# Kernel tuning notes

Hardware: AMD Instinct MI355X
Metric: run time of the kernel (lower is better)

Reference implementation:

```python
import jax, jax.numpy as jnp
import numpy as np
from jax import lax

B, T, D, NH = 8, 2048, 128, 4
HD = D // NH
EPS = 1e-5


def _ln(x, g, b):
    m = x.mean(-1, keepdims=True)
    v = ((x - m) ** 2).mean(-1, keepdims=True)
    return (x - m) / jnp.sqrt(v + EPS) * g + b


def _gelu(x):  # exact (erf) GELU, matching torch nn.GELU default
    return jax.nn.gelu(x, approximate=False)


def _forward(lob_feat, trade_feat, has_trade,
             ei_w, ei_b, ei_g, ei_beta, decay,
             in_proj_w, in_proj_b, out_proj_w, out_proj_b,
             cn_g, cn_b,
             lob_w, lob_b, lob_g, lob_beta,
             tr_w, tr_b, tr_g, tr_beta,
             of_w, of_b, of_g, of_beta):
    # event impact: Linear -> LayerNorm -> Tanh, gated by has_trade
    impact = jnp.tanh(_ln(trade_feat @ ei_w.T + ei_b, ei_g, ei_beta))
    impact = impact * has_trade[..., None]              # [B,T,D]

    # diagonal linear recurrence: state_t = sigmoid(decay) * state_{t-1} + impact_t
    d = jax.nn.sigmoid(decay)                           # [D]

    def step(s, x):
        s = d * s + x
        return s, s

    _, states = lax.scan(step, jnp.zeros_like(impact[:, 0]),
                         jnp.swapaxes(impact, 0, 1))    # [T,B,D]
    state_seq = jnp.swapaxes(states, 0, 1)              # [B,T,D]

    # fusion MLPs (dropout is identity in eval)
    lob_enh = _gelu(_ln(jnp.concatenate([lob_feat, state_seq], -1) @ lob_w.T + lob_b,
                        lob_g, lob_beta))
    trade_enh = _gelu(_ln(jnp.concatenate([trade_feat, state_seq], -1) @ tr_w.T + tr_b,
                          tr_g, tr_beta))

    # torch nn.MultiheadAttention (batch_first): q=lob_enh, k=v=trade_enh
    wq, wk, wv = in_proj_w[:D], in_proj_w[D:2 * D], in_proj_w[2 * D:]
    bq, bk, bv = in_proj_b[:D], in_proj_b[D:2 * D], in_proj_b[2 * D:]
    q = (lob_enh @ wq.T + bq).reshape(B, T, NH, HD)
    k = (trade_enh @ wk.T + bk).reshape(B, T, NH, HD)
    v = (trade_enh @ wv.T + bv).reshape(B, T, NH, HD)
    scores = jnp.einsum('bqhd,bkhd->bhqk', q, k) / jnp.sqrt(jnp.float32(HD))
    attn = jax.nn.softmax(scores, axis=-1)
    ctx = jnp.einsum('bhqk,bkhd->bqhd', attn, v).reshape(B, T, D)
    fused_attn = ctx @ out_proj_w.T + out_proj_b

    fused = _ln(lob_enh + fused_attn, cn_g, cn_b)
    output = _gelu(_ln(jnp.concatenate([fused, trade_enh], -1) @ of_w.T + of_b,
                       of_g, of_beta))
    return output


def setup_inputs() -> dict:
    key = jax.random.key(0)
    ks = jax.random.split(key, 20)
    s1 = 1.0 / np.sqrt(D)
    s2 = 1.0 / np.sqrt(2 * D)
    return {
        'lob_feat': jax.random.normal(ks[0], (B, T, D), jnp.float32),
        'trade_feat': jax.random.normal(ks[1], (B, T, D), jnp.float32),
        'has_trade': (jax.random.uniform(ks[2], (B, T)) < 0.5).astype(jnp.float32),
        'ei_w': jax.random.normal(ks[3], (D, D), jnp.float32) * s1,
        'ei_b': jnp.zeros((D,), jnp.float32),
        'ei_g': jnp.ones((D,), jnp.float32),
        'ei_beta': jnp.zeros((D,), jnp.float32),
        'decay': jnp.ones((D,), jnp.float32) * 0.9,
        'in_proj_w': jax.random.normal(ks[4], (3 * D, D), jnp.float32) * s1,
        'in_proj_b': jnp.zeros((3 * D,), jnp.float32),
        'out_proj_w': jax.random.normal(ks[5], (D, D), jnp.float32) * s1,
        'out_proj_b': jnp.zeros((D,), jnp.float32),
        'cn_g': jnp.ones((D,), jnp.float32),
        'cn_b': jnp.zeros((D,), jnp.float32),
        'lob_w': jax.random.normal(ks[6], (D, 2 * D), jnp.float32) * s2,
        'lob_b': jnp.zeros((D,), jnp.float32),
        'lob_g': jnp.ones((D,), jnp.float32),
        'lob_beta': jnp.zeros((D,), jnp.float32),
        'tr_w': jax.random.normal(ks[7], (D, 2 * D), jnp.float32) * s2,
        'tr_b': jnp.zeros((D,), jnp.float32),
        'tr_g': jnp.ones((D,), jnp.float32),
        'tr_beta': jnp.zeros((D,), jnp.float32),
        'of_w': jax.random.normal(ks[8], (D, 2 * D), jnp.float32) * s2,
        'of_b': jnp.zeros((D,), jnp.float32),
        'of_g': jnp.ones((D,), jnp.float32),
        'of_beta': jnp.zeros((D,), jnp.float32),
    }


def reference(lob_feat, trade_feat, has_trade,
              ei_w, ei_b, ei_g, ei_beta, decay,
              in_proj_w, in_proj_b, out_proj_w, out_proj_b,
              cn_g, cn_b,
              lob_w, lob_b, lob_g, lob_beta,
              tr_w, tr_b, tr_g, tr_beta,
              of_w, of_b, of_g, of_beta):
    return _forward(lob_feat, trade_feat, has_trade,
                    ei_w, ei_b, ei_g, ei_beta, decay,
                    in_proj_w, in_proj_b, out_proj_w, out_proj_b,
                    cn_g, cn_b,
                    lob_w, lob_b, lob_g, lob_beta,
                    tr_w, tr_b, tr_g, tr_beta,
                    of_w, of_b, of_g, of_beta)
```

## Files before the change

kernel.cpp:

```cpp
#include <hip/hip_runtime.h>
#include <math.h>


#define T_  2048

typedef short bf16x8 __attribute__((ext_vector_type(8)));
typedef float f32x4  __attribute__((ext_vector_type(4)));
typedef unsigned short ushort_t;

__device__ __forceinline__ float sigm(float x) { return 1.0f / (1.0f + __expf(-x)); }

__device__ __forceinline__ unsigned short f2bf(float x) {
    union { float f; unsigned u; } v; v.f = x;
    unsigned r = v.u + 0x7FFFu + ((v.u >> 16) & 1u);
    return (unsigned short)(r >> 16);
}

__global__ __launch_bounds__(256) void prep_kernel(
    const float* __restrict__ lob, const float* __restrict__ trade,
    const float* __restrict__ eiw, const float* __restrict__ ipw,
    const float* __restrict__ opw, const float* __restrict__ lobw,
    const float* __restrict__ trw, const float* __restrict__ ofw,
    ushort_t* __restrict__ pool)
{
    const size_t i8 = ((size_t)blockIdx.x * 256 + threadIdx.x) * 8;
    const float* src; size_t off;
    if      (i8 < 2097152) { src = lob;   off = 0; }
    else if (i8 < 4194304) { src = trade; off = 2097152; }
    else if (i8 < 4210688) { src = eiw;   off = 4194304; }
    else if (i8 < 4259840) { src = ipw;   off = 4210688; }
    else if (i8 < 4276224) { src = opw;   off = 4259840; }
    else if (i8 < 4308992) { src = lobw;  off = 4276224; }
    else if (i8 < 4341760) { src = trw;   off = 4308992; }
    else                   { src = ofw;   off = 4341760; }
    const float4 a = *(const float4*)(src + (i8 - off));
    const float4 b = *(const float4*)(src + (i8 - off) + 4);
    bf16x8 o;
    o[0] = (short)f2bf(a.x); o[1] = (short)f2bf(a.y);
    o[2] = (short)f2bf(a.z); o[3] = (short)f2bf(a.w);
    o[4] = (short)f2bf(b.x); o[5] = (short)f2bf(b.y);
    o[6] = (short)f2bf(b.z); o[7] = (short)f2bf(b.w);
    *(bf16x8*)(pool + i8) = o;
}

template <int KTOT, int EPI, bool WF32, bool WBF>
__global__ __launch_bounds__(256) void gemm_mfma(
    const ushort_t* __restrict__ Xb0, const ushort_t* __restrict__ Xb1,
    const ushort_t* __restrict__ Wb,
    const float* __restrict__ bias, const float* __restrict__ gamma,
    const float* __restrict__ beta, const float* __restrict__ extra,
    float* __restrict__ outf, ushort_t* __restrict__ outb)
{
    __shared__ float red[32][2][2];
    const int tid = threadIdx.x, wid = tid >> 6, lane = tid & 63;
    const int c2 = lane & 15, g = lane >> 4;
    const int rowblk = wid >> 1, chf = wid & 1, cb0 = chf * 4;
    const int R0 = blockIdx.x * 32 + rowblk * 16;

    f32x4 acc[4] = {};
#pragma unroll
    for (int ch = 0; ch < KTOT / 32; ch++) {
        const ushort_t* xs = (KTOT == 256 && ch >= 4) ? Xb1 : Xb0;
        const int kk = (KTOT == 256 && ch >= 4) ? (ch - 4) * 32 : ch * 32;
        const bf16x8 a = *(const bf16x8*)(xs + (size_t)(R0 + c2) * 128 + kk + g * 8);
#pragma unroll
        for (int j = 0; j < 4; j++) {
            const bf16x8 b = *(const bf16x8*)(Wb + (size_t)((cb0 + j) * 16 + c2) * KTOT + ch * 32 + g * 8);
            acc[j] = __builtin_amdgcn_mfma_f32_16x16x32_bf16(a, b, acc[j], 0, 0, 0);
        }
    }
    float gm[4], bt[4];
#pragma unroll
    for (int j = 0; j < 4; j++) {
        const int col = (cb0 + j) * 16 + c2;
        const float bb = bias[col];
        gm[j] = gamma[col]; bt[j] = beta[col];
#pragma unroll
        for (int r = 0; r < 4; r++) acc[j][r] += bb;
    }
    if constexpr (EPI == 2) {
#pragma unroll
        for (int j = 0; j < 4; j++)
#pragma unroll
            for (int r = 0; r < 4; r++)
                acc[j][r] += extra[(size_t)(R0 + 4 * g + r) * 128 + (cb0 + j) * 16 + c2];
    }
#pragma unroll
    for (int r = 0; r < 4; r++) {
        float s = 0.f, ss = 0.f;
#pragma unroll
        for (int j = 0; j < 4; j++) { const float v = acc[j][r]; s += v; ss = fmaf(v, v, ss); }
#pragma unroll
        for (int o = 8; o; o >>= 1) { s += __shfl_xor(s, o); ss += __shfl_xor(ss, o); }
        if (c2 == 0) {
            red[rowblk * 16 + 4 * g + r][chf][0] = s;
            red[rowblk * 16 + 4 * g + r][chf][1] = ss;
        }
    }
    __syncthreads();
#pragma unroll
    for (int r = 0; r < 4; r++) {
        const int lr = rowblk * 16 + 4 * g + r;
        const float S  = red[lr][0][0] + red[lr][1][0];
        const float SS = red[lr][0][1] + red[lr][1][1];
        const float mean = S * (1.0f / 128.0f);
        float var = SS * (1.0f / 128.0f) - mean * mean;
        var = fmaxf(var, 0.0f);
        const float rstd = rsqrtf(var + 1e-5f);
        const int R = blockIdx.x * 32 + lr;
        const float ext = (EPI == 0) ? extra[R] : 0.0f;
#pragma unroll
        for (int j = 0; j < 4; j++) {
            float y = (acc[j][r] - mean) * rstd * gm[j] + bt[j];
            if constexpr (EPI == 0) y = tanhf(y) * ext;
            if constexpr (EPI == 1) y = 0.5f * y * (1.0f + erff(y * 0.70710678118654752f));
            const int col = (cb0 + j) * 16 + c2;
            if constexpr (WF32) outf[(size_t)R * 128 + col] = y;
            if constexpr (WBF)  outb[(size_t)R * 128 + col] = f2bf(y);
        }
    }
}

__global__ __launch_bounds__(256) void gemm_dual(
    const ushort_t* __restrict__ XA0, const ushort_t* __restrict__ XB0,
    const ushort_t* __restrict__ X1,
    const ushort_t* __restrict__ WA, const ushort_t* __restrict__ WB,
    const float* __restrict__ biasA, const float* __restrict__ biasB,
    const float* __restrict__ gA, const float* __restrict__ gB,
    const float* __restrict__ bA, const float* __restrict__ bB,
    float* __restrict__ outfA, ushort_t* __restrict__ outbA, ushort_t* __restrict__ outbB)
{
    __shared__ float red[32][2][2];
    const int sel = blockIdx.y;
    const ushort_t* Xb0 = sel ? XB0 : XA0;
    const ushort_t* Wb  = sel ? WB  : WA;
    const float* bias = sel ? biasB : biasA;
    const float* gamma = sel ? gB : gA;
    const float* beta  = sel ? bB : bA;
    ushort_t* outb = sel ? outbB : outbA;

    const int tid = threadIdx.x, wid = tid >> 6, lane = tid & 63;
    const int c2 = lane & 15, g = lane >> 4;
    const int rowblk = wid >> 1, chf = wid & 1, cb0 = chf * 4;
    const int R0 = blockIdx.x * 32 + rowblk * 16;

    f32x4 acc[4] = {};
#pragma unroll
    for (int ch = 0; ch < 8; ch++) {
        const ushort_t* xs = (ch >= 4) ? X1 : Xb0;
        const int kk = (ch >= 4) ? (ch - 4) * 32 : ch * 32;
        const bf16x8 a = *(const bf16x8*)(xs + (size_t)(R0 + c2) * 128 + kk + g * 8);
#pragma unroll
        for (int j = 0; j < 4; j++) {
            const bf16x8 b = *(const bf16x8*)(Wb + (size_t)((cb0 + j) * 16 + c2) * 256 + ch * 32 + g * 8);
            acc[j] = __builtin_amdgcn_mfma_f32_16x16x32_bf16(a, b, acc[j], 0, 0, 0);
        }
    }
    float gm[4], bt[4];
#pragma unroll
    for (int j = 0; j < 4; j++) {
        const int col = (cb0 + j) * 16 + c2;
        const float bb = bias[col];
        gm[j] = gamma[col]; bt[j] = beta[col];
#pragma unroll
        for (int r = 0; r < 4; r++) acc[j][r] += bb;
    }
#pragma unroll
    for (int r = 0; r < 4; r++) {
        float s = 0.f, ss = 0.f;
#pragma unroll
        for (int j = 0; j < 4; j++) { const float v = acc[j][r]; s += v; ss = fmaf(v, v, ss); }
#pragma unroll
        for (int o = 8; o; o >>= 1) { s += __shfl_xor(s, o); ss += __shfl_xor(ss, o); }
        if (c2 == 0) {
            red[rowblk * 16 + 4 * g + r][chf][0] = s;
            red[rowblk * 16 + 4 * g + r][chf][1] = ss;
        }
    }
    __syncthreads();
#pragma unroll
    for (int r = 0; r < 4; r++) {
        const int lr = rowblk * 16 + 4 * g + r;
        const float S  = red[lr][0][0] + red[lr][1][0];
        const float SS = red[lr][0][1] + red[lr][1][1];
        const float mean = S * (1.0f / 128.0f);
        float var = SS * (1.0f / 128.0f) - mean * mean;
        var = fmaxf(var, 0.0f);
        const float rstd = rsqrtf(var + 1e-5f);
        const int R = blockIdx.x * 32 + lr;
#pragma unroll
        for (int j = 0; j < 4; j++) {
            float y = (acc[j][r] - mean) * rstd * gm[j] + bt[j];
            y = 0.5f * y * (1.0f + erff(y * 0.70710678118654752f));
            const int col = (cb0 + j) * 16 + c2;
            if (!sel) outfA[(size_t)R * 128 + col] = y;
            outb[(size_t)R * 128 + col] = f2bf(y);
        }
    }
}

__global__ __launch_bounds__(256) void qkv_mfma(
    const ushort_t* __restrict__ lobe, const ushort_t* __restrict__ tre,
    const ushort_t* __restrict__ ipw, const float* __restrict__ ipb,
    ushort_t* __restrict__ qo, ushort_t* __restrict__ ko, ushort_t* __restrict__ vo)
{
    __shared__ ushort_t vls[128][36];
    const int tid = threadIdx.x, wid = tid >> 6, lane = tid & 63;
    const int c2 = lane & 15, g = lane >> 4;
    const int rowblk = wid >> 1, chf = wid & 1, cb0 = chf * 4;
    const int RB = blockIdx.x * 32;
    const int R0 = RB + rowblk * 16;
    const int which = blockIdx.y;
    const ushort_t* X = (which == 0) ? lobe : tre;
    const ushort_t* Wp = ipw + (size_t)which * 16384;

    f32x4 acc[4] = {};
#pragma unroll
    for (int ch = 0; ch < 4; ch++) {
        const bf16x8 a = *(const bf16x8*)(X + (size_t)(R0 + c2) * 128 + ch * 32 + g * 8);
#pragma unroll
        for (int j = 0; j < 4; j++) {
            const bf16x8 b = *(const bf16x8*)(Wp + (size_t)((cb0 + j) * 16 + c2) * 128 + ch * 32 + g * 8);
            acc[j] = __builtin_amdgcn_mfma_f32_16x16x32_bf16(a, b, acc[j], 0, 0, 0);
        }
    }
    const float qscale = 0.17677669529663687f * 1.4426950408889634f;
    if (which < 2) {
        ushort_t* dst = (which == 0) ? qo : ko;
        const float sc = (which == 0) ? qscale : 1.0f;
#pragma unroll
        for (int j = 0; j < 4; j++) {
            const int col = (cb0 + j) * 16 + c2;
            const float bb = ipb[which * 128 + col];
            const int h = col >> 5, hd = col & 31;
#pragma unroll
            for (int r = 0; r < 4; r++) {
                const int R = R0 + 4 * g + r;
                const int b = R >> 11, t = R & 2047;
                dst[(((size_t)b * 4 + h) * 2048 + t) * 32 + hd] = f2bf((acc[j][r] + bb) * sc);
            }
        }
    } else {
#pragma unroll
        for (int j = 0; j < 4; j++) {
            const int col = (cb0 + j) * 16 + c2;
            const float bb = ipb[256 + col];
#pragma unroll
            for (int r = 0; r < 4; r++)
                vls[col][rowblk * 16 + 4 * g + r] = f2bf(acc[j][r] + bb);
        }
        __syncthreads();
        const int col = tid >> 1, hf = tid & 1;
        const int h = col >> 5, hd = col & 31;
        const int b = RB >> 11;
        unsigned w[8];
#pragma unroll
        for (int e = 0; e < 8; e++) w[e] = *(const unsigned*)&vls[col][hf * 16 + e * 2];
        ushort_t* dst = vo + (((size_t)b * 4 + h) * 32 + hd) * 2048 + (RB & 2047) + hf * 16;
        *(uint4*)dst       = *(const uint4*)&w[0];
        *(uint4*)(dst + 8) = *(const uint4*)&w[4];
    }
}

__global__ __launch_bounds__(256) void attn_kernel(
    const ushort_t* __restrict__ q, const ushort_t* __restrict__ k,
    const ushort_t* __restrict__ vtg, ushort_t* __restrict__ ctx)
{
    __shared__ ushort_t ks[2][64][40];
    __shared__ ushort_t vt[2][32][72];
    __shared__ ushort_t ps[64][72];
    const int tid = threadIdx.x, wid = tid >> 6, lane = tid & 63;
    const int c = lane & 15, g = lane >> 4;
    const int qt = blockIdx.x, bh = blockIdx.y, b = bh >> 2, h = bh & 3;
    const ushort_t* kb_ = k   + (size_t)bh * 65536;
    const ushort_t* vb_ = vtg + (size_t)bh * 65536;

    const bf16x8 qf = *(const bf16x8*)(q + ((size_t)bh * 2048 + qt * 64 + wid * 16 + c) * 32 + g * 8);

    float m_i[4], rs_[4];
    f32x4 acc[2] = {};
#pragma unroll
    for (int r = 0; r < 4; r++) { m_i[r] = 8.0f; rs_[r] = 0.0f; }

    const int srow = tid >> 2, ssg = tid & 3;
    const int vd = tid >> 3, vkg = tid & 7;

    {
        const bf16x8 kk8 = *(const bf16x8*)(kb_ + (size_t)srow * 32 + ssg * 8);
        const bf16x8 vv8 = *(const bf16x8*)(vb_ + (size_t)vd * 2048 + vkg * 8);
        *(bf16x8*)&ks[0][srow][ssg * 8] = kk8;
        *(bf16x8*)&vt[0][vd][vkg * 8] = vv8;
    }
    __syncthreads();

    for (int kt = 0; kt < 32; kt++) {
        const int cur = kt & 1;
        bf16x8 kk8, vv8;
        if (kt + 1 < 32) {
            kk8 = *(const bf16x8*)(kb_ + ((size_t)(kt + 1) * 64 + srow) * 32 + ssg * 8);
            vv8 = *(const bf16x8*)(vb_ + (size_t)vd * 2048 + (kt + 1) * 64 + vkg * 8);
        }

        f32x4 s[4];
#pragma unroll
        for (int kb2 = 0; kb2 < 4; kb2++) {
            const bf16x8 kf = *(const bf16x8*)&ks[cur][kb2 * 16 + c][g * 8];
            f32x4 z = {};
            s[kb2] = __builtin_amdgcn_mfma_f32_16x16x32_bf16(qf, kf, z, 0, 0, 0);
        }

        int need = 0;
        float lmax[4];
#pragma unroll
        for (int r = 0; r < 4; r++) {
            lmax[r] = fmaxf(fmaxf(s[0][r], s[1][r]), fmaxf(s[2][r], s[3][r]));
            need |= (lmax[r] > m_i[r] + 40.0f) ? 1 : 0;
        }
        if (__any(need)) {
#pragma unroll
            for (int r = 0; r < 4; r++) {
                float tm = lmax[r];
#pragma unroll
                for (int o = 8; o; o >>= 1) tm = fmaxf(tm, __shfl_xor(tm, o));
                const float mn = fmaxf(m_i[r], tm);
                const float al = exp2f(m_i[r] - mn);
                rs_[r] *= al; acc[0][r] *= al; acc[1][r] *= al;
                m_i[r] = mn;
            }
        }

#pragma unroll
        for (int r = 0; r < 4; r++) {
            const float p0 = exp2f(s[0][r] - m_i[r]);
            const float p1 = exp2f(s[1][r] - m_i[r]);
            const float p2 = exp2f(s[2][r] - m_i[r]);
            const float p3 = exp2f(s[3][r] - m_i[r]);
            rs_[r] += (p0 + p1) + (p2 + p3);
            unsigned w01, w23;
            asm("v_cvt_pk_bf16_f32 %0, %1, %2" : "=v"(w01) : "v"(p0), "v"(p1));
            asm("v_cvt_pk_bf16_f32 %0, %1, %2" : "=v"(w23) : "v"(p2), "v"(p3));
            ushort_t* prow = &ps[wid * 16 + 4 * g + r][c];
            prow[0]  = (ushort_t)w01;
            prow[16] = (ushort_t)(w01 >> 16);
            prow[32] = (ushort_t)w23;
            prow[48] = (ushort_t)(w23 >> 16);
        }

        const bf16x8 pa0 = *(const bf16x8*)&ps[wid * 16 + c][g * 8];
        const bf16x8 pa1 = *(const bf16x8*)&ps[wid * 16 + c][32 + g * 8];
#pragma unroll
        for (int nb = 0; nb < 2; nb++) {
            const bf16x8 v0 = *(const bf16x8*)&vt[cur][nb * 16 + c][g * 8];
            const bf16x8 v1 = *(const bf16x8*)&vt[cur][nb * 16 + c][32 + g * 8];
            acc[nb] = __builtin_amdgcn_mfma_f32_16x16x32_bf16(pa0, v0, acc[nb], 0, 0, 0);
            acc[nb] = __builtin_amdgcn_mfma_f32_16x16x32_bf16(pa1, v1, acc[nb], 0, 0, 0);
        }

        if (kt + 1 < 32) {
            *(bf16x8*)&ks[cur ^ 1][srow][ssg * 8] = kk8;
            *(bf16x8*)&vt[cur ^ 1][vd][vkg * 8] = vv8;
        }
        __syncthreads();
    }

#pragma unroll
    for (int r = 0; r < 4; r++) {
        float t = rs_[r];
#pragma unroll
        for (int o = 8; o; o >>= 1) t += __shfl_xor(t, o);
        const float inv = 1.0f / t;
        const int tq = qt * 64 + wid * 16 + 4 * g + r;
        ushort_t* dst = ctx + ((size_t)(b * 2048 + tq)) * 128 + h * 32;
        dst[c]      = f2bf(acc[0][r] * inv);
        dst[16 + c] = f2bf(acc[1][r] * inv);
    }
}

__global__ void scan_local_kernel(float* __restrict__ st, const float* __restrict__ decay)
{
    const int c = threadIdx.x;
    const int ch = blockIdx.x, b = blockIdx.y;
    const float d = sigm(decay[c]);
    const size_t base = ((size_t)b * T_ + ch * 64) * 128 + c;
    float s = 0.0f;
#pragma unroll 4
    for (int tl = 0; tl < 64; tl++) {
        const float x = st[base + (size_t)tl * 128];
        s = fmaf(d, s, x);
        st[base + (size_t)tl * 128] = s;
    }
}

__global__ void scan_carry_kernel(const float* __restrict__ st, const float* __restrict__ decay,
                                  float* __restrict__ carry)
{
    const int c = threadIdx.x;
    const int b = blockIdx.x;
    const float d = sigm(decay[c]);
    float dl = d;
#pragma unroll
    for (int i = 0; i < 6; i++) dl *= dl;
    float ends[32];
#pragma unroll
    for (int ch = 0; ch < 32; ch++)
        ends[ch] = st[((size_t)b * T_ + ch * 64 + 63) * 128 + c];
    float e = 0.0f;
#pragma unroll
    for (int ch = 0; ch < 32; ch++) {
        carry[((size_t)b * 32 + ch) * 128 + c] = e;
        e = fmaf(dl, e, ends[ch]);
    }
}

__global__ void scan_fin_kernel(const float* __restrict__ st, const float* __restrict__ decay,
                                const float* __restrict__ carry, ushort_t* __restrict__ stbf)
{
    const int c = threadIdx.x;
    const int ch = blockIdx.x, b = blockIdx.y;
    const float d = sigm(decay[c]);
    const float cr = ch ? carry[((size_t)b * 32 + ch) * 128 + c] : 0.0f;
    const size_t base = ((size_t)b * T_ + ch * 64) * 128 + c;
    float p = d;
#pragma unroll 4
    for (int tl = 0; tl < 64; tl++) {
        const float s2 = st[base + (size_t)tl * 128] + p * cr;
        p *= d;
        stbf[base + (size_t)tl * 128] = f2bf(s2);
    }
}

extern "C" void kernel_launch(void* const* d_in, const int* in_sizes, int n_in,
                              void* d_out, int out_size, void* d_ws, size_t ws_size,
                              hipStream_t stream)
{
    const float* lob_feat   = (const float*)d_in[0];
    const float* trade_feat = (const float*)d_in[1];
    const float* has_trade  = (const float*)d_in[2];
    const float* ei_w       = (const float*)d_in[3];
    const float* ei_b       = (const float*)d_in[4];
    const float* ei_g       = (const float*)d_in[5];
    const float* ei_beta    = (const float*)d_in[6];
    const float* decay      = (const float*)d_in[7];
    const float* in_proj_w  = (const float*)d_in[8];
    const float* in_proj_b  = (const float*)d_in[9];
    const float* out_proj_w = (const float*)d_in[10];
    const float* out_proj_b = (const float*)d_in[11];
    const float* cn_g       = (const float*)d_in[12];
    const float* cn_b       = (const float*)d_in[13];
    const float* lob_w      = (const float*)d_in[14];
    const float* lob_b      = (const float*)d_in[15];
    const float* lob_g      = (const float*)d_in[16];
    const float* lob_beta   = (const float*)d_in[17];
    const float* tr_w       = (const float*)d_in[18];
    const float* tr_b       = (const float*)d_in[19];
    const float* tr_g       = (const float*)d_in[20];
    const float* tr_beta    = (const float*)d_in[21];
    const float* of_w       = (const float*)d_in[22];
    const float* of_b       = (const float*)d_in[23];
    const float* of_g       = (const float*)d_in[24];
    const float* of_beta    = (const float*)d_in[25];

    char* W = (char*)d_ws;
    const size_t MB = 1u << 20;
    float*    state_f  = (float*)W;
    float*    lobe_f   = state_f;
    float*    carry    = (float*)(W + 8 * MB);
    ushort_t* pool     = (ushort_t*)(W + 9 * MB);
    ushort_t* state_bf = (ushort_t*)(W + 18 * MB);
    ushort_t* lobe_bf  = (ushort_t*)(W + 22 * MB);
    ushort_t* tre_bf   = (ushort_t*)(W + 26 * MB);
    ushort_t* q_bf     = (ushort_t*)(W + 30 * MB);
    ushort_t* k_bf     = (ushort_t*)(W + 34 * MB);
    ushort_t* vt_g     = (ushort_t*)(W + 38 * MB);
    ushort_t* ctx_bf   = (ushort_t*)(W + 42 * MB);
    ushort_t* fused_bf = (ushort_t*)(W + 46 * MB);

    ushort_t* lob_bf   = pool;
    ushort_t* trade_bf = pool + 2097152;
    ushort_t* eiw_bf   = pool + 4194304;
    ushort_t* ipw_bf   = pool + 4210688;
    ushort_t* opw_bf   = pool + 4259840;
    ushort_t* lobw_bf  = pool + 4276224;
    ushort_t* trw_bf   = pool + 4308992;
    ushort_t* ofw_bf   = pool + 4341760;

    const dim3 blk(256);

    prep_kernel<<<dim3(2136), blk, 0, stream>>>(lob_feat, trade_feat, ei_w, in_proj_w,
                                                out_proj_w, lob_w, tr_w, of_w, pool);
    gemm_mfma<128, 0, true, false><<<dim3(512), blk, 0, stream>>>(
        trade_bf, nullptr, eiw_bf, ei_b, ei_g, ei_beta, has_trade, state_f, nullptr);
    scan_local_kernel<<<dim3(32, 8), dim3(128), 0, stream>>>(state_f, decay);
    scan_carry_kernel<<<dim3(8), dim3(128), 0, stream>>>(state_f, decay, carry);
    scan_fin_kernel<<<dim3(32, 8), dim3(128), 0, stream>>>(state_f, decay, carry, state_bf);
    gemm_dual<<<dim3(512, 2), blk, 0, stream>>>(
        lob_bf, trade_bf, state_bf, lobw_bf, trw_bf, lob_b, tr_b,
        lob_g, tr_g, lob_beta, tr_beta, lobe_f, lobe_bf, tre_bf);
    qkv_mfma<<<dim3(512, 3), blk, 0, stream>>>(lobe_bf, tre_bf, ipw_bf, in_proj_b,
                                               q_bf, k_bf, vt_g);
    attn_kernel<<<dim3(32, 32), blk, 0, stream>>>(q_bf, k_bf, vt_g, ctx_bf);
    gemm_mfma<128, 2, false, true><<<dim3(512), blk, 0, stream>>>(
        ctx_bf, nullptr, opw_bf, out_proj_b, cn_g, cn_b, lobe_f, nullptr, fused_bf);
    gemm_mfma<256, 1, true, false><<<dim3(512), blk, 0, stream>>>(
        fused_bf, tre_bf, ofw_bf, of_b, of_g, of_beta, nullptr, (float*)d_out, nullptr);
}
```

Baseline: 163.4 us.

## Fuse enhancement MLPs with QKV and out-proj with final MLP, fast activations

Merges the lob/trade fusion MLPs with the QKV projection in one kernel, keeping the enhanced rows in LDS, and merges out-projection, residual LayerNorm and the final MLP into another. This removes intermediate global writes and reads and several launches. It also replaces erf GELU and tanhf with exp2/rcp-based approximations, adds s_setprio around MFMA blocks in attention, and packs P stores with the V layout permuted to match. The GELU approximation trades exactness for cheaper math.

Result: faster. 149.4 us (-8.6%).

```diff
diff --git a/kernel.cpp b/kernel.cpp
--- a/kernel.cpp
+++ b/kernel.cpp
@@ -14,6 +14,15 @@
     union { float f; unsigned u; } v; v.f = x;
     unsigned r = v.u + 0x7FFFu + ((v.u >> 16) & 1u);
     return (unsigned short)(r >> 16);
+}
+
+__device__ __forceinline__ float gelu_f(float x) {
+    const float e = exp2f(fmaf(0.044715f * x, x * x, x) * -2.3022083f);
+    return x * __builtin_amdgcn_rcpf(1.0f + e);
+}
+__device__ __forceinline__ float tanh_f(float y) {
+    const float e = exp2f(y * 2.8853900818f);
+    return 1.0f - 2.0f * __builtin_amdgcn_rcpf(e + 1.0f);
 }
 
 __global__ __launch_bounds__(256) void prep_kernel(
@@ -43,13 +52,11 @@
     *(bf16x8*)(pool + i8) = o;
 }
 
-template <int KTOT, int EPI, bool WF32, bool WBF>
-__global__ __launch_bounds__(256) void gemm_mfma(
-    const ushort_t* __restrict__ Xb0, const ushort_t* __restrict__ Xb1,
-    const ushort_t* __restrict__ Wb,
+__global__ __launch_bounds__(256) void gemm_ei(
+    const ushort_t* __restrict__ Xb0, const ushort_t* __restrict__ Wb,
     const float* __restrict__ bias, const float* __restrict__ gamma,
     const float* __restrict__ beta, const float* __restrict__ extra,
-    float* __restrict__ outf, ushort_t* __restrict__ outb)
+    float* __restrict__ outf)
 {
     __shared__ float red[32][2][2];
     const int tid = threadIdx.x, wid = tid >> 6, lane = tid & 63;
@@ -59,13 +66,11 @@
 
     f32x4 acc[4] = {};
 #pragma unroll
-    for (int ch = 0; ch < KTOT / 32; ch++) {
-        const ushort_t* xs = (KTOT == 256 && ch >= 4) ? Xb1 : Xb0;
-        const int kk = (KTOT == 256 && ch >= 4) ? (ch - 4) * 32 : ch * 32;
-        const bf16x8 a = *(const bf16x8*)(xs + (size_t)(R0 + c2) * 128 + kk + g * 8);
-#pragma unroll
-        for (int j = 0; j < 4; j++) {
-            const bf16x8 b = *(const bf16x8*)(Wb + (size_t)((cb0 + j) * 16 + c2) * KTOT + ch * 32 + g * 8);
+    for (int ch = 0; ch < 4; ch++) {
+        const bf16x8 a = *(const bf16x8*)(Xb0 + (size_t)(R0 + c2) * 128 + ch * 32 + g * 8);
+#pragma unroll
+        for (int j = 0; j < 4; j++) {
+            const bf16x8 b = *(const bf16x8*)(Wb + (size_t)((cb0 + j) * 16 + c2) * 128 + ch * 32 + g * 8);
             acc[j] = __builtin_amdgcn_mfma_f32_16x16x32_bf16(a, b, acc[j], 0, 0, 0);
         }
     }
@@ -77,13 +82,6 @@
         gm[j] = gamma[col]; bt[j] = beta[col];
 #pragma unroll
         for (int r = 0; r < 4; r++) acc[j][r] += bb;
-    }
-    if constexpr (EPI == 2) {
-#pragma unroll
-        for (int j = 0; j < 4; j++)
-#pragma unroll
-            for (int r = 0; r < 4; r++)
-                acc[j][r] += extra[(size_t)(R0 + 4 * g + r) * 128 + (cb0 + j) * 16 + c2];
     }
 #pragma unroll
     for (int r = 0; r < 4; r++) {
@@ -108,154 +106,160 @@
         var = fmaxf(var, 0.0f);
         const float rstd = rsqrtf(var + 1e-5f);
         const int R = blockIdx.x * 32 + lr;
-        const float ext = (EPI == 0) ? extra[R] : 0.0f;
-#pragma unroll
-        for (int j = 0; j < 4; j++) {
-            float y = (acc[j][r] - mean) * rstd * gm[j] + bt[j];
-            if constexpr (EPI == 0) y = tanhf(y) * ext;
-            if constexpr (EPI == 1) y = 0.5f * y * (1.0f + erff(y * 0.70710678118654752f));
-            const int col = (cb0 + j) * 16 + c2;
-            if constexpr (WF32) outf[(size_t)R * 128 + col] = y;
-            if constexpr (WBF)  outb[(size_t)R * 128 + col] = f2bf(y);
-        }
-    }
-}
-
-__global__ __launch_bounds__(256) void gemm_dual(
-    const ushort_t* __restrict__ XA0, const ushort_t* __restrict__ XB0,
-    const ushort_t* __restrict__ X1,
-    const ushort_t* __restrict__ WA, const ushort_t* __restrict__ WB,
-    const float* __restrict__ biasA, const float* __restrict__ biasB,
-    const float* __restrict__ gA, const float* __restrict__ gB,
-    const float* __restrict__ bA, const float* __restrict__ bB,
-    float* __restrict__ outfA, ushort_t* __restrict__ outbA, ushort_t* __restrict__ outbB)
-{
-    __shared__ float red[32][2][2];
-    const int sel = blockIdx.y;
-    const ushort_t* Xb0 = sel ? XB0 : XA0;
-    const ushort_t* Wb  = sel ? WB  : WA;
-    const float* bias = sel ? biasB : biasA;
-    const float* gamma = sel ? gB : gA;
-    const float* beta  = sel ? bB : bA;
-    ushort_t* outb = sel ? outbB : outbA;
-
-    const int tid = threadIdx.x, wid = tid >> 6, lane = tid & 63;
-    const int c2 = lane & 15, g = lane >> 4;
-    const int rowblk = wid >> 1, chf = wid & 1, cb0 = chf * 4;
-    const int R0 = blockIdx.x * 32 + rowblk * 16;
-
-    f32x4 acc[4] = {};
-#pragma unroll
-    for (int ch = 0; ch < 8; ch++) {
-        const ushort_t* xs = (ch >= 4) ? X1 : Xb0;
-        const int kk = (ch >= 4) ? (ch - 4) * 32 : ch * 32;
-        const bf16x8 a = *(const bf16x8*)(xs + (size_t)(R0 + c2) * 128 + kk + g * 8);
-#pragma unroll
-        for (int j = 0; j < 4; j++) {
-            const bf16x8 b = *(const bf16x8*)(Wb + (size_t)((cb0 + j) * 16 + c2) * 256 + ch * 32 + g * 8);
-            acc[j] = __builtin_amdgcn_mfma_f32_16x16x32_bf16(a, b, acc[j], 0, 0, 0);
-        }
-    }
-    float gm[4], bt[4];
-#pragma unroll
-    for (int j = 0; j < 4; j++) {
-        const int col = (cb0 + j) * 16 + c2;
-        const float bb = bias[col];
-        gm[j] = gamma[col]; bt[j] = beta[col];
-#pragma unroll
-        for (int r = 0; r < 4; r++) acc[j][r] += bb;
-    }
-#pragma unroll
-    for (int r = 0; r < 4; r++) {
-        float s = 0.f, ss = 0.f;
-#pragma unroll
-        for (int j = 0; j < 4; j++) { const float v = acc[j][r]; s += v; ss = fmaf(v, v, ss); }
-#pragma unroll
-        for (int o = 8; o; o >>= 1) { s += __shfl_xor(s, o); ss += __shfl_xor(ss, o); }
-        if (c2 == 0) {
-            red[rowblk * 16 + 4 * g + r][chf][0] = s;
-            red[rowblk * 16 + 4 * g + r][chf][1] = ss;
-        }
-    }
-    __syncthreads();
-#pragma unroll
-    for (int r = 0; r < 4; r++) {
-        const int lr = rowblk * 16 + 4 * g + r;
-        const float S  = red[lr][0][0] + red[lr][1][0];
-        const float SS = red[lr][0][1] + red[lr][1][1];
-        const float mean = S * (1.0f / 128.0f);
-        float var = SS * (1.0f / 128.0f) - mean * mean;
-        var = fmaxf(var, 0.0f);
-        const float rstd = rsqrtf(var + 1e-5f);
-        const int R = blockIdx.x * 32 + lr;
-#pragma unroll
-        for (int j = 0; j < 4; j++) {
-            float y = (acc[j][r] - mean) * rstd * gm[j] + bt[j];
-            y = 0.5f * y * (1.0f + erff(y * 0.70710678118654752f));
-            const int col = (cb0 + j) * 16 + c2;
-            if (!sel) outfA[(size_t)R * 128 + col] = y;
-            outb[(size_t)R * 128 + col] = f2bf(y);
-        }
-    }
-}
-
-__global__ __launch_bounds__(256) void qkv_mfma(
-    const ushort_t* __restrict__ lobe, const ushort_t* __restrict__ tre,
+        const float ext = extra[R];
+#pragma unroll
+        for (int j = 0; j < 4; j++) {
+            const float y = (acc[j][r] - mean) * rstd * gm[j] + bt[j];
+            outf[(size_t)R * 128 + (cb0 + j) * 16 + c2] = tanh_f(y) * ext;
+        }
+    }
+}
+
+__global__ __launch_bounds__(256) void enh_qkv(
+    const ushort_t* __restrict__ lobb, const ushort_t* __restrict__ trab,
+    const ushort_t* __restrict__ stab,
+    const ushort_t* __restrict__ lobw, const ushort_t* __restrict__ trw,
     const ushort_t* __restrict__ ipw, const float* __restrict__ ipb,
+    const float* __restrict__ lob_b, const float* __restrict__ lob_g,
+    const float* __restrict__ lob_beta,
+    const float* __restrict__ tr_b, const float* __restrict__ tr_g,
+    const float* __restrict__ tr_beta,
+    float* __restrict__ lobe_f, ushort_t* __restrict__ tre_bf,
     ushort_t* __restrict__ qo, ushort_t* __restrict__ ko, ushort_t* __restrict__ vo)
 {
+    __shared__ ushort_t lob_t[32][136];
+    __shared__ ushort_t tre_t[32][136];
     __shared__ ushort_t vls[128][36];
+    __shared__ float red[32][2][4];
     const int tid = threadIdx.x, wid = tid >> 6, lane = tid & 63;
     const int c2 = lane & 15, g = lane >> 4;
     const int rowblk = wid >> 1, chf = wid & 1, cb0 = chf * 4;
     const int RB = blockIdx.x * 32;
     const int R0 = RB + rowblk * 16;
-    const int which = blockIdx.y;
-    const ushort_t* X = (which == 0) ? lobe : tre;
-    const ushort_t* Wp = ipw + (size_t)which * 16384;
-
-    f32x4 acc[4] = {};
-#pragma unroll
-    for (int ch = 0; ch < 4; ch++) {
-        const bf16x8 a = *(const bf16x8*)(X + (size_t)(R0 + c2) * 128 + ch * 32 + g * 8);
-#pragma unroll
-        for (int j = 0; j < 4; j++) {
-            const bf16x8 b = *(const bf16x8*)(Wp + (size_t)((cb0 + j) * 16 + c2) * 128 + ch * 32 + g * 8);
-            acc[j] = __builtin_amdgcn_mfma_f32_16x16x32_bf16(a, b, acc[j], 0, 0, 0);
-        }
-    }
+
+    f32x4 aL[4] = {}, aT[4] = {};
+#pragma unroll
+    for (int ch = 0; ch < 8; ch++) {
+        const int kk = (ch & 3) * 32;
+        bf16x8 xl, xt;
+        if (ch < 4) {
+            xl = *(const bf16x8*)(lobb + (size_t)(R0 + c2) * 128 + kk + g * 8);
+            xt = *(const bf16x8*)(trab + (size_t)(R0 + c2) * 128 + kk + g * 8);
+        } else {
+            xl = *(const bf16x8*)(stab + (size_t)(R0 + c2) * 128 + kk + g * 8);
+            xt = xl;
+        }
+#pragma unroll
+        for (int j = 0; j < 4; j++) {
+            const size_t wo = (size_t)((cb0 + j) * 16 + c2) * 256 + ch * 32 + g * 8;
+            aL[j] = __builtin_amdgcn_mfma_f32_16x16x32_bf16(xl, *(const bf16x8*)(lobw + wo), aL[j], 0, 0, 0);
+            aT[j] = __builtin_amdgcn_mfma_f32_16x16x32_bf16(xt, *(const bf16x8*)(trw + wo), aT[j], 0, 0, 0);
+        }
+    }
+#pragma unroll
+    for (int j = 0; j < 4; j++) {
+        const int col = (cb0 + j) * 16 + c2;
+        const float bL = lob_b[col], bT = tr_b[col];
+#pragma unroll
+        for (int r = 0; r < 4; r++) { aL[j][r] += bL; aT[j][r] += bT; }
+    }
+#pragma unroll
+    for (int r = 0; r < 4; r++) {
+        float sL = 0.f, ssL = 0.f, sT = 0.f, ssT = 0.f;
+#pragma unroll
+        for (int j = 0; j < 4; j++) {
+            const float vL = aL[j][r], vT = aT[j][r];
+            sL += vL; ssL = fmaf(vL, vL, ssL);
+            sT += vT; ssT = fmaf(vT, vT, ssT);
+        }
+#pragma unroll
+        for (int o = 8; o; o >>= 1) {
+            sL += __shfl_xor(sL, o); ssL += __shfl_xor(ssL, o);
+            sT += __shfl_xor(sT, o); ssT += __shfl_xor(ssT, o);
+        }
+        if (c2 == 0) {
+            float* rd = red[rowblk * 16 + 4 * g + r][chf];
+            rd[0] = sL; rd[1] = ssL; rd[2] = sT; rd[3] = ssT;
+        }
+    }
+    __syncthreads();
+#pragma unroll
+    for (int r = 0; r < 4; r++) {
+        const int lr = rowblk * 16 + 4 * g + r;
+        const int R = RB + lr;
+        const float SL  = red[lr][0][0] + red[lr][1][0];
+        const float SSL = red[lr][0][1] + red[lr][1][1];
+        const float ST  = red[lr][0][2] + red[lr][1][2];
+        const float SST = red[lr][0][3] + red[lr][1][3];
+        const float mL = SL * (1.0f / 128.0f), mT = ST * (1.0f / 128.0f);
+        const float rL = rsqrtf(fmaxf(SSL * (1.0f / 128.0f) - mL * mL, 0.0f) + 1e-5f);
+        const float rT = rsqrtf(fmaxf(SST * (1.0f / 128.0f) - mT * mT, 0.0f) + 1e-5f);
+#pragma unroll
+        for (int j = 0; j < 4; j++) {
+            const int col = (cb0 + j) * 16 + c2;
+            const float yL = gelu_f((aL[j][r] - mL) * rL * lob_g[col] + lob_beta[col]);
+            const float yT = gelu_f((aT[j][r] - mT) * rT * tr_g[col] + tr_beta[col]);
+            lobe_f[(size_t)R * 128 + col] = yL;
+            lob_t[lr][col] = f2bf(yL);
+            const ushort_t tb = f2bf(yT);
+            tre_bf[(size_t)R * 128 + col] = tb;
+            tre_t[lr][col] = tb;
+        }
+    }
+    __syncthreads();
+
     const float qscale = 0.17677669529663687f * 1.4426950408889634f;
-    if (which < 2) {
-        ushort_t* dst = (which == 0) ? qo : ko;
-        const float sc = (which == 0) ? qscale : 1.0f;
-#pragma unroll
-        for (int j = 0; j < 4; j++) {
-            const int col = (cb0 + j) * 16 + c2;
-            const float bb = ipb[which * 128 + col];
-            const int h = col >> 5, hd = col & 31;
-#pragma unroll
-            for (int r = 0; r < 4; r++) {
-                const int R = R0 + 4 * g + r;
-                const int b = R >> 11, t = R & 2047;
-                dst[(((size_t)b * 4 + h) * 2048 + t) * 32 + hd] = f2bf((acc[j][r] + bb) * sc);
+#pragma unroll
+    for (int which = 0; which < 3; which++) {
+        const ushort_t (*src)[136] = (which == 0) ? lob_t : tre_t;
+        const ushort_t* Wp = ipw + (size_t)which * 16384;
+        f32x4 pa[4] = {};
+#pragma unroll
+        for (int ch = 0; ch < 4; ch++) {
+            const bf16x8 a = *(const bf16x8*)&src[rowblk * 16 + c2][ch * 32 + g * 8];
+#pragma unroll
+            for (int j = 0; j < 4; j++) {
+                const bf16x8 b = *(const bf16x8*)(Wp + (size_t)((cb0 + j) * 16 + c2) * 128 + ch * 32 + g * 8);
+                pa[j] = __builtin_amdgcn_mfma_f32_16x16x32_bf16(a, b, pa[j], 0, 0, 0);
             }
         }
-    } else {
-#pragma unroll
-        for (int j = 0; j < 4; j++) {
-            const int col = (cb0 + j) * 16 + c2;
-            const float bb = ipb[256 + col];
-#pragma unroll
-            for (int r = 0; r < 4; r++)
-                vls[col][rowblk * 16 + 4 * g + r] = f2bf(acc[j][r] + bb);
-        }
-        __syncthreads();
+        if (which < 2) {
+            ushort_t* dst = (which == 0) ? qo : ko;
+            const float sc = (which == 0) ? qscale : 1.0f;
+#pragma unroll
+            for (int j = 0; j < 4; j++) {
+                const int col = (cb0 + j) * 16 + c2;
+                const float bb = ipb[which * 128 + col];
+                const int h = col >> 5, hd = col & 31;
+#pragma unroll
+                for (int r = 0; r < 4; r++) {
+                    const int R = R0 + 4 * g + r;
+                    const int b = R >> 11, t = R & 2047;
+                    dst[(((size_t)b * 4 + h) * 2048 + t) * 32 + hd] = f2bf((pa[j][r] + bb) * sc);
+                }
+            }
+        } else {
+#pragma unroll
+            for (int j = 0; j < 4; j++) {
+                const int col = (cb0 + j) * 16 + c2;
+                const float bb = ipb[256 + col];
+#pragma unroll
+                for (int r = 0; r < 4; r++)
+                    vls[col][rowblk * 16 + 4 * g + r] = f2bf(pa[j][r] + bb);
+            }
+        }
+    }
+    __syncthreads();
+    {
         const int col = tid >> 1, hf = tid & 1;
         const int h = col >> 5, hd = col & 31;
         const int b = RB >> 11;
         unsigned w[8];
 #pragma unroll
-        for (int e = 0; e < 8; e++) w[e] = *(const unsigned*)&vls[col][hf * 16 + e * 2];
+        for (int e = 0; e < 8; e++) {
+            const int cp = hf * 8 + e;
+            w[e] = (unsigned)vls[col][cp] | ((unsigned)vls[col][cp + 16] << 16);
+        }
         ushort_t* dst = vo + (((size_t)b * 4 + h) * 32 + hd) * 2048 + (RB & 2047) + hf * 16;
         *(uint4*)dst       = *(const uint4*)&w[0];
         *(uint4*)(dst + 8) = *(const uint4*)&w[4];
@@ -302,12 +306,14 @@
         }
 
         f32x4 s[4];
+        __builtin_amdgcn_s_setprio(1);
 #pragma unroll
         for (int kb2 = 0; kb2 < 4; kb2++) {
             const bf16x8 kf = *(const bf16x8*)&ks[cur][kb2 * 16 + c][g * 8];
             f32x4 z = {};
             s[kb2] = __builtin_amdgcn_mfma_f32_16x16x32_bf16(qf, kf, z, 0, 0, 0);
         }
+        __builtin_amdgcn_s_setprio(0);
 
         int need = 0;
         float lmax[4];
@@ -339,15 +345,14 @@
             unsigned w01, w23;
             asm("v_cvt_pk_bf16_f32 %0, %1, %2" : "=v"(w01) : "v"(p0), "v"(p1));
             asm("v_cvt_pk_bf16_f32 %0, %1, %2" : "=v"(w23) : "v"(p2), "v"(p3));
-            ushort_t* prow = &ps[wid * 16 + 4 * g + r][c];
-            prow[0]  = (ushort_t)w01;
-            prow[16] = (ushort_t)(w01 >> 16);
-            prow[32] = (ushort_t)w23;
-            prow[48] = (ushort_t)(w23 >> 16);
+            ushort_t* prow = ps[wid * 16 + 4 * g + r];
+            *(unsigned*)&prow[2 * c] = w01;
+            *(unsigned*)&prow[32 + 2 * c] = w23;
         }
 
         const bf16x8 pa0 = *(const bf16x8*)&ps[wid * 16 + c][g * 8];
         const bf16x8 pa1 = *(const bf16x8*)&ps[wid * 16 + c][32 + g * 8];
+        __builtin_amdgcn_s_setprio(1);
 #pragma unroll
         for (int nb = 0; nb < 2; nb++) {
             const bf16x8 v0 = *(const bf16x8*)&vt[cur][nb * 16 + c][g * 8];
@@ -355,6 +360,7 @@
             acc[nb] = __builtin_amdgcn_mfma_f32_16x16x32_bf16(pa0, v0, acc[nb], 0, 0, 0);
             acc[nb] = __builtin_amdgcn_mfma_f32_16x16x32_bf16(pa1, v1, acc[nb], 0, 0, 0);
         }
+        __builtin_amdgcn_s_setprio(0);
 
         if (kt + 1 < 32) {
             *(bf16x8*)&ks[cur ^ 1][srow][ssg * 8] = kk8;
@@ -368,11 +374,121 @@
         float t = rs_[r];
 #pragma unroll
         for (int o = 8; o; o >>= 1) t += __shfl_xor(t, o);
-        const float inv = 1.0f / t;
+        const float inv = __builtin_amdgcn_rcpf(t);
         const int tq = qt * 64 + wid * 16 + 4 * g + r;
         ushort_t* dst = ctx + ((size_t)(b * 2048 + tq)) * 128 + h * 32;
         dst[c]      = f2bf(acc[0][r] * inv);
         dst[16 + c] = f2bf(acc[1][r] * inv);
+    }
+}
+
+__global__ __launch_bounds__(256) void out_fuse(
+    const ushort_t* __restrict__ ctxb, const ushort_t* __restrict__ treb,
+    const ushort_t* __restrict__ opw, const float* __restrict__ opb,
+    const float* __restrict__ cn_g, const float* __restrict__ cn_b,
+    const ushort_t* __restrict__ ofw, const float* __restrict__ of_b,
+    const float* __restrict__ of_g, const float* __restrict__ of_beta,
+    const float* __restrict__ lobe_f, float* __restrict__ out)
+{
+    __shared__ ushort_t fus_t[32][136];
+    __shared__ float red[32][2][2];
+    const int tid = threadIdx.x, wid = tid >> 6, lane = tid & 63;
+    const int c2 = lane & 15, g = lane >> 4;
+    const int rowblk = wid >> 1, chf = wid & 1, cb0 = chf * 4;
+    const int RB = blockIdx.x * 32;
+    const int R0 = RB + rowblk * 16;
+
+    f32x4 acc[4] = {};
+#pragma unroll
+    for (int ch = 0; ch < 4; ch++) {
+        const bf16x8 a = *(const bf16x8*)(ctxb + (size_t)(R0 + c2) * 128 + ch * 32 + g * 8);
+#pragma unroll
+        for (int j = 0; j < 4; j++) {
+            const bf16x8 b = *(const bf16x8*)(opw + (size_t)((cb0 + j) * 16 + c2) * 128 + ch * 32 + g * 8);
+            acc[j] = __builtin_amdgcn_mfma_f32_16x16x32_bf16(a, b, acc[j], 0, 0, 0);
+        }
+    }
+#pragma unroll
+    for (int j = 0; j < 4; j++) {
+        const int col = (cb0 + j) * 16 + c2;
+        const float bb = opb[col];
+#pragma unroll
+        for (int r = 0; r < 4; r++)
+            acc[j][r] += bb + lobe_f[(size_t)(R0 + 4 * g + r) * 128 + col];
+    }
+#pragma unroll
+    for (int r = 0; r < 4; r++) {
+        float s = 0.f, ss = 0.f;
+#pragma unroll
+        for (int j = 0; j < 4; j++) { const float v = acc[j][r]; s += v; ss = fmaf(v, v, ss); }
+#pragma unroll
+        for (int o = 8; o; o >>= 1) { s += __shfl_xor(s, o); ss += __shfl_xor(ss, o); }
+        if (c2 == 0) {
+            red[rowblk * 16 + 4 * g + r][chf][0] = s;
+            red[rowblk * 16 + 4 * g + r][chf][1] = ss;
+        }
+    }
+    __syncthreads();
+#pragma unroll
+    for (int r = 0; r < 4; r++) {
+        const int lr = rowblk * 16 + 4 * g + r;
+        const float S  = red[lr][0][0] + red[lr][1][0];
+        const float SS = red[lr][0][1] + red[lr][1][1];
+        const float mean = S * (1.0f / 128.0f);
+        const float rstd = rsqrtf(fmaxf(SS * (1.0f / 128.0f) - mean * mean, 0.0f) + 1e-5f);
+#pragma unroll
+        for (int j = 0; j < 4; j++) {
+            const int col = (cb0 + j) * 16 + c2;
+            fus_t[lr][col] = f2bf((acc[j][r] - mean) * rstd * cn_g[col] + cn_b[col]);
+        }
+    }
+    __syncthreads();
+
+    f32x4 a2[4] = {};
+#pragma unroll
+    for (int ch = 0; ch < 8; ch++) {
+        bf16x8 a;
+        if (ch < 4) a = *(const bf16x8*)&fus_t[rowblk * 16 + c2][ch * 32 + g * 8];
+        else        a = *(const bf16x8*)(treb + (size_t)(R0 + c2) * 128 + (ch - 4) * 32 + g * 8);
+#pragma unroll
+        for (int j = 0; j < 4; j++) {
+            const bf16x8 b = *(const bf16x8*)(ofw + (size_t)((cb0 + j) * 16 + c2) * 256 + ch * 32 + g * 8);
+            a2[j] = __builtin_amdgcn_mfma_f32_16x16x32_bf16(a, b, a2[j], 0, 0, 0);
+        }
+    }
+#pragma unroll
+    for (int j = 0; j < 4; j++) {
+        const float bb = of_b[(cb0 + j) * 16 + c2];
+#pragma unroll
+        for (int r = 0; r < 4; r++) a2[j][r] += bb;
+    }
+#pragma unroll
+    for (int r = 0; r < 4; r++) {
+        float s = 0.f, ss = 0.f;
+#pragma unroll
+        for (int j = 0; j < 4; j++) { const float v = a2[j][r]; s += v; ss = fmaf(v, v, ss); }
+#pragma unroll
+        for (int o = 8; o; o >>= 1) { s += __shfl_xor(s, o); ss += __shfl_xor(ss, o); }
+        if (c2 == 0) {
+            red[rowblk * 16 + 4 * g + r][chf][0] = s;
+            red[rowblk * 16 + 4 * g + r][chf][1] = ss;
+        }
+    }
+    __syncthreads();
+#pragma unroll
+    for (int r = 0; r < 4; r++) {
+        const int lr = rowblk * 16 + 4 * g + r;
+        const float S  = red[lr][0][0] + red[lr][1][0];
+        const float SS = red[lr][0][1] + red[lr][1][1];
+        const float mean = S * (1.0f / 128.0f);
+        const float rstd = rsqrtf(fmaxf(SS * (1.0f / 128.0f) - mean * mean, 0.0f) + 1e-5f);
+        const int R = RB + lr;
+#pragma unroll
+        for (int j = 0; j < 4; j++) {
+            const int col = (cb0 + j) * 16 + c2;
+            const float y = (a2[j][r] - mean) * rstd * of_g[col] + of_beta[col];
+            out[(size_t)R * 128 + col] = gelu_f(y);
+        }
     }
 }
 
@@ -467,13 +583,11 @@
     float*    carry    = (float*)(W + 8 * MB);
     ushort_t* pool     = (ushort_t*)(W + 9 * MB);
     ushort_t* state_bf = (ushort_t*)(W + 18 * MB);
-    ushort_t* lobe_bf  = (ushort_t*)(W + 22 * MB);
     ushort_t* tre_bf   = (ushort_t*)(W + 26 * MB);
     ushort_t* q_bf     = (ushort_t*)(W + 30 * MB);
     ushort_t* k_bf     = (ushort_t*)(W + 34 * MB);
     ushort_t* vt_g     = (ushort_t*)(W + 38 * MB);
     ushort_t* ctx_bf   = (ushort_t*)(W + 42 * MB);
-    ushort_t* fused_bf = (ushort_t*)(W + 46 * MB);
 
     ushort_t* lob_bf   = pool;
     ushort_t* trade_bf = pool + 2097152;
@@ -488,19 +602,16 @@
 
     prep_kernel<<<dim3(2136), blk, 0, stream>>>(lob_feat, trade_feat, ei_w, in_proj_w,
                                                 out_proj_w, lob_w, tr_w, of_w, pool);
-    gemm_mfma<128, 0, true, false><<<dim3(512), blk, 0, stream>>>(
-        trade_bf, nullptr, eiw_bf, ei_b, ei_g, ei_beta, has_trade, state_f, nullptr);
+    gemm_ei<<<dim3(512), blk, 0, stream>>>(trade_bf, eiw_bf, ei_b, ei_g, ei_beta,
+                                           has_trade, state_f);
     scan_local_kernel<<<dim3(32, 8), dim3(128), 0, stream>>>(state_f, decay);
     scan_carry_kernel<<<dim3(8), dim3(128), 0, stream>>>(state_f, decay, carry);
     scan_fin_kernel<<<dim3(32, 8), dim3(128), 0, stream>>>(state_f, decay, carry, state_bf);
-    gemm_dual<<<dim3(512, 2), blk, 0, stream>>>(
-        lob_bf, trade_bf, state_bf, lobw_bf, trw_bf, lob_b, tr_b,
-        lob_g, tr_g, lob_beta, tr_beta, lobe_f, lobe_bf, tre_bf);
-    qkv_mfma<<<dim3(512, 3), blk, 0, stream>>>(lobe_bf, tre_bf, ipw_bf, in_proj_b,
-                                               q_bf, k_bf, vt_g);
+    enh_qkv<<<dim3(512), blk, 0, stream>>>(lob_bf, trade_bf, state_bf, lobw_bf, trw_bf,
+                                           ipw_bf, in_proj_b, lob_b, lob_g, lob_beta,
+                                           tr_b, tr_g, tr_beta, lobe_f, tre_bf,
+                                           q_bf, k_bf, vt_g);
     attn_kernel<<<dim3(32, 32), blk, 0, stream>>>(q_bf, k_bf, vt_g, ctx_bf);
-    gemm_mfma<128, 2, false, true><<<dim3(512), blk, 0, stream>>>(
-        ctx_bf, nullptr, opw_bf, out_proj_b, cn_g, cn_b, lobe_f, nullptr, fused_bf);
-    gemm_mfma<256, 1, true, false><<<dim3(512), blk, 0, stream>>>(
-        fused_bf, tre_bf, ofw_bf, of_b, of_g, of_beta, nullptr, (float*)d_out, nullptr);
-}
+    out_fuse<<<dim3(512), blk, 0, stream>>>(ctx_bf, tre_bf, opw_bf, out_proj_b, cn_g, cn_b,
+                                            ofw_bf, of_b, of_g, of_beta, lobe_f, (float*)d_out);
+}
```
